# Optimization experiments

Measured on AMD Instinct MI355X. Metric: run time of the kernel, lower is better.

The kernel has to match this reference:

```python
import jax, jax.numpy as jnp
import numpy as np

FX, FY, CX, CY = 300.0, 300.0, 128.0, 128.0
W, H = 256, 256
NEAR, FAR = 0.01, 100.0
MAX_RADIUS = 64.0
N_GAUSS = 512


def _quat_to_rot(q):
    # (N,4) wxyz quaternion -> (N,3,3) rotation matrix
    q = q / jnp.linalg.norm(q, axis=-1, keepdims=True)
    w, x, y, z = q[..., 0], q[..., 1], q[..., 2], q[..., 3]
    R = jnp.stack([1 - 2 * y * y - 2 * z * z, 2 * x * y - 2 * w * z, 2 * x * z + 2 * w * y,
                   2 * x * y + 2 * w * z, 1 - 2 * x * x - 2 * z * z, 2 * y * z - 2 * w * x,
                   2 * x * z - 2 * w * y, 2 * y * z + 2 * w * x, 1 - 2 * x * x - 2 * y * y], axis=-1)
    return R.reshape(q.shape[:-1] + (3, 3))


def _render(positions, scales, rotations, colors, opacities, view_matrix):
    N = positions.shape[0]
    homo = jnp.concatenate([positions, jnp.ones((N, 1), positions.dtype)], axis=1)
    pc = jnp.einsum('ij,nj->ni', view_matrix, homo)[:, :3]  # camera-space points
    depths = -pc[:, 2]
    R = _quat_to_rot(rotations)
    S = jnp.eye(3, dtype=scales.dtype)[None] * scales[:, None, :]  # diag_embed
    RS = jnp.einsum('ij,njk,nkl->nil', view_matrix[:3, :3], R, S)
    cov3d = RS @ jnp.swapaxes(RS, -1, -2)
    x, y, z = pc[:, 0], pc[:, 1], pc[:, 2]
    z_safe = jnp.maximum(jnp.abs(z), 0.01) * jnp.sign(z + 1e-8)
    z2 = z_safe * z_safe
    zero = jnp.zeros_like(z)
    # Jacobian of perspective projection (N,2,3), signs as in the torch source
    J = jnp.stack([jnp.stack([FX / -z_safe, zero, FX * x / z2], axis=-1),
                   jnp.stack([zero, FY / z_safe, FY * y / z2], axis=-1)], axis=1)
    cov2d = jnp.einsum('nij,njk,nlk->nil', J, cov3d, J)
    u = FX * x / -z_safe + CX
    v = FY * -y / -z_safe + CY
    mx, my = u, v
    # effective radius: 3 * sqrt(max eigenvalue), clamped
    a, b = cov2d[:, 0, 0], cov2d[:, 0, 1]
    c, d = cov2d[:, 1, 0], cov2d[:, 1, 1]
    trace = a + d
    det = jnp.maximum(a * d - b * c, 1e-6)
    disc = jnp.maximum(trace * trace - 4 * det, 0.0)
    lam = (trace + jnp.sqrt(disc)) / 2
    radii = jnp.minimum(3.0 * jnp.sqrt(jnp.maximum(lam, 1e-6)), MAX_RADIUS)
    # front-to-back depth sort
    order = jnp.argsort(depths)
    mx, my = mx[order], my[order]
    cov2d = cov2d[order]
    colors_s = colors[order]
    opac_s = opacities[order]
    depths_s = depths[order]
    radii_s = radii[order]
    visible = ((depths_s > NEAR) & (depths_s < FAR)
               & (mx + radii_s > 0) & (mx - radii_s < W)
               & (my + radii_s > 0) & (my - radii_s < H))
    cov_reg = cov2d + 1e-4 * jnp.eye(2, dtype=cov2d.dtype)
    ra, rb = cov_reg[:, 0, 0], cov_reg[:, 0, 1]
    rc, rd = cov_reg[:, 1, 0], cov_reg[:, 1, 1]
    rdet = ra * rd - rb * rc
    ia, ib, ic, id_ = rd / rdet, -rb / rdet, -rc / rdet, ra / rdet
    px = jnp.arange(W, dtype=jnp.float32)
    py = jnp.arange(H, dtype=jnp.float32)
    # per-Gaussian bounding window, matching torch int() truncation
    x0 = jnp.maximum(0.0, jnp.trunc(mx - radii_s))
    x1 = jnp.minimum(float(W), jnp.trunc(mx + radii_s) + 1.0)
    y0 = jnp.maximum(0.0, jnp.trunc(my - radii_s))
    y1 = jnp.minimum(float(H), jnp.trunc(my + radii_s) + 1.0)
    in_x = (px[None, :] >= x0[:, None]) & (px[None, :] < x1[:, None])  # (N,W)
    in_y = (py[None, :] >= y0[:, None]) & (py[None, :] < y1[:, None])  # (N,H)
    mask = in_y[:, :, None] & in_x[:, None, :] & visible[:, None, None]  # (N,H,W)
    dx = px[None, None, :] - mx[:, None, None]  # (N,1,W)->(N,H,W) broadcast
    dy = py[None, :, None] - my[:, None, None]
    m = (ia[:, None, None] * dx * dx + (ib + ic)[:, None, None] * dx * dy
         + id_[:, None, None] * dy * dy)
    gauss = jnp.exp(-0.5 * m)
    alpha = jnp.where(mask, jnp.clip(opac_s[:, None, None] * gauss, 0.0, 0.99), 0.0)
    # over-compositing: weight_i = alpha_i * prod_{j<i}(1 - alpha_j)
    T = jnp.concatenate([jnp.ones((1, H, W), alpha.dtype),
                         jnp.cumprod(1.0 - alpha, axis=0)[:-1]], axis=0)
    wgt = alpha * T
    img = jnp.einsum('nhw,nc->chw', wgt, colors_s)
    bg = jnp.zeros((3,), img.dtype)  # background = (0,0,0)
    img = img + bg[:, None, None] * (1.0 - jnp.sum(wgt, axis=0))[None]
    return img  # (3,H,W)


def setup_inputs() -> dict:
    key = jax.random.key(0)
    k = jax.random.split(key, 6)
    xy = jax.random.uniform(k[0], (N_GAUSS, 2), minval=-3.0, maxval=3.0)
    z = jax.random.uniform(k[1], (N_GAUSS, 1), minval=-10.0, maxval=-2.0)  # in front of camera
    positions = jnp.concatenate([xy, z], axis=1)
    scales = jax.random.uniform(k[2], (N_GAUSS, 3), minval=0.02, maxval=0.15)
    rotations = jax.random.normal(k[3], (N_GAUSS, 4))
    colors = jax.random.uniform(k[4], (N_GAUSS, 3))
    opacities = jax.random.uniform(k[5], (N_GAUSS,), minval=0.05, maxval=0.95)
    view_matrix = jnp.eye(4, dtype=jnp.float32)
    return {"positions": positions, "scales": scales, "rotations": rotations,
            "colors": colors, "opacities": opacities, "view_matrix": view_matrix}


def reference(positions, scales, rotations, colors, opacities, view_matrix):
    return _render(positions, scales, rotations, colors, opacities, view_matrix)
```

## Files before the change

kernel.cpp:

```cpp
#include <hip/hip_runtime.h>
#include <math.h>

#define NG     512
#define IMG_W  256
#define IMG_H  256
#define FXc    300.0f
#define FYc    300.0f
#define CXc    128.0f
#define CYc    128.0f
#define NEARc  0.01f
#define FARc   100.0f
#define MAXR   64.0f

struct GParam {
  float mx, my, ia, ibc;
  float idv, opac, cr, cg;
  float cb, x0, x1, y0;
  float y1, depth, pad1, pad2;
};

__device__ __forceinline__ unsigned int ordered_float(float f) {
  unsigned int u = __float_as_uint(f);
  return (u & 0x80000000u) ? ~u : (u | 0x80000000u);
}

__global__ __launch_bounds__(1024, 4) void fused_render_kernel(
    const float* __restrict__ pos, const float* __restrict__ scl,
    const float* __restrict__ rot, const float* __restrict__ col,
    const float* __restrict__ opa, const float* __restrict__ vm,
    float* __restrict__ out)
{
  __shared__ GParam sg[NG];
  __shared__ unsigned long long keys[NG];
  __shared__ short order[NG];
  __shared__ int wave_cnt[8];

  const int t = threadIdx.x;
  const int wid = t >> 6;
  const int lane = t & 63;

  float V[12];
#pragma unroll
  for (int k = 0; k < 12; ++k) V[k] = vm[k];

  if (t < NG) {
    const int i = t;

    const float p0 = pos[i*3+0], p1 = pos[i*3+1], p2 = pos[i*3+2];
    const float pcx = V[0]*p0 + V[1]*p1 + V[2]*p2  + V[3];
    const float pcy = V[4]*p0 + V[5]*p1 + V[6]*p2  + V[7];
    const float pcz = V[8]*p0 + V[9]*p1 + V[10]*p2 + V[11];
    const float depth = -pcz;

    float qw = rot[i*4+0], qx = rot[i*4+1], qy = rot[i*4+2], qz = rot[i*4+3];
    const float qinv = 1.f / sqrtf(qw*qw + qx*qx + qy*qy + qz*qz);
    qw *= qinv; qx *= qinv; qy *= qinv; qz *= qinv;
    const float r00 = 1.f - 2.f*(qy*qy + qz*qz);
    const float r01 = 2.f*(qx*qy - qw*qz);
    const float r02 = 2.f*(qx*qz + qw*qy);
    const float r10 = 2.f*(qx*qy + qw*qz);
    const float r11 = 1.f - 2.f*(qx*qx + qz*qz);
    const float r12 = 2.f*(qy*qz - qw*qx);
    const float r20 = 2.f*(qx*qz - qw*qy);
    const float r21 = 2.f*(qy*qz + qw*qx);
    const float r22 = 1.f - 2.f*(qx*qx + qy*qy);

    const float s0 = scl[i*3+0], s1 = scl[i*3+1], s2 = scl[i*3+2];

    const float m00 = V[0]*r00 + V[1]*r10 + V[2]*r20;
    const float m01 = V[0]*r01 + V[1]*r11 + V[2]*r21;
    const float m02 = V[0]*r02 + V[1]*r12 + V[2]*r22;
    const float m10 = V[4]*r00 + V[5]*r10 + V[6]*r20;
    const float m11 = V[4]*r01 + V[5]*r11 + V[6]*r21;
    const float m12 = V[4]*r02 + V[5]*r12 + V[6]*r22;
    const float m20 = V[8]*r00 + V[9]*r10 + V[10]*r20;
    const float m21 = V[8]*r01 + V[9]*r11 + V[10]*r21;
    const float m22 = V[8]*r02 + V[9]*r12 + V[10]*r22;

    const float a0 = m00*s0, a1 = m01*s1, a2 = m02*s2;
    const float b0 = m10*s0, b1 = m11*s1, b2 = m12*s2;
    const float c0 = m20*s0, c1 = m21*s1, c2 = m22*s2;
    const float c00 = a0*a0 + a1*a1 + a2*a2;
    const float c01 = a0*b0 + a1*b1 + a2*b2;
    const float c02 = a0*c0 + a1*c1 + a2*c2;
    const float c11 = b0*b0 + b1*b1 + b2*b2;
    const float c12 = b0*c0 + b1*c1 + b2*c2;
    const float c22 = c0*c0 + c1*c1 + c2*c2;

    const float zp = pcz + 1e-8f;
    const float sgn = (zp > 0.f) ? 1.f : ((zp < 0.f) ? -1.f : 0.f);
    const float z_safe = fmaxf(fabsf(pcz), 0.01f) * sgn;
    const float rz2 = 1.f / (z_safe * z_safe);
    const float rnz = 1.f / (-z_safe);

    const float j00 = FXc * rnz;
    const float j02 = FXc * pcx * rz2;
    const float j11 = FYc * (-rnz);
    const float j12 = FYc * pcy * rz2;

    const float t00 = j00*c00 + j02*c02;
    const float t01 = j00*c01 + j02*c12;
    const float t02 = j00*c02 + j02*c22;
    const float t10 = j11*c01 + j12*c02;
    const float t11 = j11*c11 + j12*c12;
    const float t12 = j11*c12 + j12*c22;
    const float ca  = t00*j00 + t02*j02;
    const float cbv = t01*j11 + t02*j12;
    const float cc  = t10*j00 + t12*j02;
    const float cd  = t11*j11 + t12*j12;

    const float u = FXc * pcx * rnz + CXc;
    const float v = FYc * (-pcy) * rnz + CYc;

    const float trace = ca + cd;
    const float det = fmaxf(ca*cd - cbv*cc, 1e-6f);
    const float disc = fmaxf(trace*trace - 4.f*det, 0.f);
    const float lam = (trace + sqrtf(disc)) * 0.5f;
    const float radii = fminf(3.f * sqrtf(fmaxf(lam, 1e-6f)), MAXR);

    const bool visible = (depth > NEARc) && (depth < FARc) &&
                         (u + radii > 0.f) && (u - radii < (float)IMG_W) &&
                         (v + radii > 0.f) && (v - radii < (float)IMG_H);

    const float ra = ca + 1e-4f;
    const float rb = cbv;
    const float rc = cc;
    const float rd = cd + 1e-4f;
    const float inv_rdet = 1.f / (ra*rd - rb*rc);

    float x0 = fmaxf(0.f, truncf(u - radii));
    float x1 = fminf((float)IMG_W, truncf(u + radii) + 1.f);
    float y0 = fmaxf(0.f, truncf(v - radii));
    float y1 = fminf((float)IMG_H, truncf(v + radii) + 1.f);
    if (!visible) { x0 = 1e9f; x1 = -1e9f; y0 = 1e9f; y1 = -1e9f; }

    GParam g;
    g.mx = u; g.my = v; g.ia = rd * inv_rdet; g.ibc = -(rb + rc) * inv_rdet;
    g.idv = ra * inv_rdet; g.opac = opa[i]; g.cr = col[i*3+0]; g.cg = col[i*3+1];
    g.cb = col[i*3+2]; g.x0 = x0; g.x1 = x1; g.y0 = y0;
    g.y1 = y1; g.depth = depth; g.pad1 = 0.f; g.pad2 = 0.f;
    sg[i] = g;
  }
  __syncthreads();

  const int tileX = blockIdx.x % (IMG_W / 16);
  const int tileY = blockIdx.x / (IMG_W / 16);
  const float tx0 = (float)(tileX * 16), tx1 = tx0 + 16.f;
  const float ty0 = (float)(tileY * 16), ty1 = ty0 + 16.f;

  bool pred = false;
  unsigned long long mb = 0;
  if (wid < 8) {
    const int g = wid * 64 + lane;
    pred = (sg[g].x0 < tx1) & (sg[g].x1 > tx0) &
           (sg[g].y0 < ty1) & (sg[g].y1 > ty0);
    mb = __ballot(pred);
    if (lane == 0) wave_cnt[wid] = __popcll(mb);
  }
  __syncthreads();

  int off = 0, total = 0;
#pragma unroll
  for (int w = 0; w < 8; ++w) {
    const int c = wave_cnt[w];
    if (w < wid) off += c;
    total += c;
  }
  if (pred) {
    const int g = wid * 64 + lane;
    const int p = off + __popcll(mb & ((1ull << lane) - 1ull));
    keys[p] = ((unsigned long long)ordered_float(sg[g].depth) << 32)
            | (unsigned int)g;
  }
  __syncthreads();

  if (t < total) {
    const unsigned long long kj = keys[t];
    int rank = 0;
    int i = 0;
    for (; i + 4 <= total; i += 4) {
      rank += (keys[i]   < kj);
      rank += (keys[i+1] < kj);
      rank += (keys[i+2] < kj);
      rank += (keys[i+3] < kj);
    }
    for (; i < total; ++i) rank += (keys[i] < kj);
    order[rank] = (short)(kj & 0xFFFFull);
  }
  __syncthreads();

  const int p = t >> 2;
  const int seg = t & 3;
  const int lx = p & 15, ly = p >> 4;
  const int px = tileX * 16 + lx;
  const int py = tileY * 16 + ly;
  const float fpx = (float)px, fpy = (float)py;

  const int L = (total + 3) >> 2;
  const int k0 = seg * L;
  const int k1 = min(k0 + L, total);

  float T = 1.f, accr = 0.f, accg = 0.f, accb = 0.f;

  for (int k = k0; k < k1; ++k) {
    const int n = (int)order[k];
    const float dx = fpx - sg[n].mx;
    const float dy = fpy - sg[n].my;
    const float m = sg[n].ia*dx*dx + sg[n].ibc*dx*dy + sg[n].idv*dy*dy;
    const float g = __expf(-0.5f * m);
    const bool in = (fpx >= sg[n].x0) & (fpx < sg[n].x1) &
                    (fpy >= sg[n].y0) & (fpy < sg[n].y1);
    float a = fminf(sg[n].opac * g, 0.99f);
    a = in ? a : 0.f;
    const float w = a * T;
    accr = fmaf(w, sg[n].cr, accr);
    accg = fmaf(w, sg[n].cg, accg);
    accb = fmaf(w, sg[n].cb, accb);
    T *= (1.f - a);
  }

  {
    float pT = __shfl_xor(T, 1);
    float pr = __shfl_xor(accr, 1);
    float pg = __shfl_xor(accg, 1);
    float pb = __shfl_xor(accb, 1);
    if (seg & 1) { accr = pr + pT*accr; accg = pg + pT*accg; accb = pb + pT*accb; }
    else         { accr = accr + T*pr;  accg = accg + T*pg;  accb = accb + T*pb; }
    T *= pT;

    pT = __shfl_xor(T, 2);
    pr = __shfl_xor(accr, 2);
    pg = __shfl_xor(accg, 2);
    pb = __shfl_xor(accb, 2);
    if (seg & 2) { accr = pr + pT*accr; accg = pg + pT*accg; accb = pb + pT*accb; }
    else         { accr = accr + T*pr;  accg = accg + T*pg;  accb = accb + T*pb; }
    T *= pT;
  }

  if (seg == 0) {
    const int pix = py * IMG_W + px;
    out[0*IMG_W*IMG_H + pix] = accr;
    out[1*IMG_W*IMG_H + pix] = accg;
    out[2*IMG_W*IMG_H + pix] = accb;
  }
}

extern "C" void kernel_launch(void* const* d_in, const int* in_sizes, int n_in,
                              void* d_out, int out_size, void* d_ws, size_t ws_size,
                              hipStream_t stream) {
  const float* pos = (const float*)d_in[0];
  const float* scl = (const float*)d_in[1];
  const float* rot = (const float*)d_in[2];
  const float* col = (const float*)d_in[3];
  const float* opa = (const float*)d_in[4];
  const float* vm  = (const float*)d_in[5];

  const int tiles = (IMG_W / 16) * (IMG_H / 16);
  fused_render_kernel<<<tiles, 1024, 0, stream>>>(pos, scl, rot, col, opa, vm,
                                                  (float*)d_out);
}
```

Measured before the change: 11.79 us.

## Use 16x8 tiles with eight depth segments per pixel

Halves the tile height so 512 blocks are launched instead of 256, and splits each pixel's sorted Gaussian list across 8 threads instead of 4, merging partial front-to-back results with a three-step shuffle tree. The aim is more blocks to fill the GPU's compute units and shorter serial per-thread blend loops. In exchange, every block still recomputes all 512 Gaussian projections and the sort, so that redundant preprocessing doubles. The launch bound minimum-blocks hint is also raised.

```diff
diff --git a/kernel.cpp b/kernel.cpp
--- a/kernel.cpp
+++ b/kernel.cpp
@@ -12,6 +12,9 @@
 #define FARc   100.0f
 #define MAXR   64.0f
 
+#define TILE_W 16
+#define TILE_H 8
+
 struct GParam {
   float mx, my, ia, ibc;
   float idv, opac, cr, cg;
@@ -24,7 +27,7 @@
   return (u & 0x80000000u) ? ~u : (u | 0x80000000u);
 }
 
-__global__ __launch_bounds__(1024, 4) void fused_render_kernel(
+__global__ __launch_bounds__(1024, 8) void fused_render_kernel(
     const float* __restrict__ pos, const float* __restrict__ scl,
     const float* __restrict__ rot, const float* __restrict__ col,
     const float* __restrict__ opa, const float* __restrict__ vm,
@@ -143,10 +146,10 @@
   }
   __syncthreads();
 
-  const int tileX = blockIdx.x % (IMG_W / 16);
-  const int tileY = blockIdx.x / (IMG_W / 16);
-  const float tx0 = (float)(tileX * 16), tx1 = tx0 + 16.f;
-  const float ty0 = (float)(tileY * 16), ty1 = ty0 + 16.f;
+  const int tileX = blockIdx.x & 15;
+  const int tileY = blockIdx.x >> 4;
+  const float tx0 = (float)(tileX * TILE_W), tx1 = tx0 + (float)TILE_W;
+  const float ty0 = (float)(tileY * TILE_H), ty1 = ty0 + (float)TILE_H;
 
   bool pred = false;
   unsigned long long mb = 0;
@@ -189,14 +192,13 @@
   }
   __syncthreads();
 
-  const int p = t >> 2;
-  const int seg = t & 3;
-  const int lx = p & 15, ly = p >> 4;
-  const int px = tileX * 16 + lx;
-  const int py = tileY * 16 + ly;
+  const int p = t >> 3;
+  const int seg = t & 7;
+  const int px = tileX * TILE_W + (p & 15);
+  const int py = tileY * TILE_H + (p >> 4);
   const float fpx = (float)px, fpy = (float)py;
 
-  const int L = (total + 3) >> 2;
+  const int L = (total + 7) >> 3;
   const int k0 = seg * L;
   const int k1 = min(k0 + L, total);
 
@@ -219,20 +221,13 @@
     T *= (1.f - a);
   }
 
-  {
-    float pT = __shfl_xor(T, 1);
-    float pr = __shfl_xor(accr, 1);
-    float pg = __shfl_xor(accg, 1);
-    float pb = __shfl_xor(accb, 1);
-    if (seg & 1) { accr = pr + pT*accr; accg = pg + pT*accg; accb = pb + pT*accb; }
-    else         { accr = accr + T*pr;  accg = accg + T*pg;  accb = accb + T*pb; }
-    T *= pT;
-
-    pT = __shfl_xor(T, 2);
-    pr = __shfl_xor(accr, 2);
-    pg = __shfl_xor(accg, 2);
-    pb = __shfl_xor(accb, 2);
-    if (seg & 2) { accr = pr + pT*accr; accg = pg + pT*accg; accb = pb + pT*accb; }
+#pragma unroll
+  for (int j = 1; j <= 4; j <<= 1) {
+    const float pT = __shfl_xor(T, j);
+    const float pr = __shfl_xor(accr, j);
+    const float pg = __shfl_xor(accg, j);
+    const float pb = __shfl_xor(accb, j);
+    if (seg & j) { accr = pr + pT*accr; accg = pg + pT*accg; accb = pb + pT*accb; }
     else         { accr = accr + T*pr;  accg = accg + T*pg;  accb = accb + T*pb; }
     T *= pT;
   }
@@ -255,7 +250,7 @@
   const float* opa = (const float*)d_in[4];
   const float* vm  = (const float*)d_in[5];
 
-  const int tiles = (IMG_W / 16) * (IMG_H / 16);
+  const int tiles = (IMG_W / TILE_W) * (IMG_H / TILE_H);
   fused_render_kernel<<<tiles, 1024, 0, stream>>>(pos, scl, rot, col, opa, vm,
                                                   (float*)d_out);
 }
```

After: 13.77 us. +16.8%, slower.
